# Performance work log

Measured on AMD Instinct MI355X. Metric: run time of the kernel, lower is better.

## Reference

```python
import jax, jax.numpy as jnp
import numpy as np

TOP_K = 2

def setup_inputs() -> dict:
    key = jax.random.key(0)
    ks = jax.random.split(key, 6)
    B, S, D, F, E = 2, 2048, 1024, 4096, 8
    sd = 1.0 / np.sqrt(D)
    sf = 1.0 / np.sqrt(F)
    return {
        "x": jax.random.normal(ks[0], (B, S, D), jnp.float32),
        "gate_w": jax.random.normal(ks[1], (D, E), jnp.float32) * sd,
        "w1": jax.random.normal(ks[2], (E, D, F), jnp.float32) * sd,
        "b1": jax.random.normal(ks[3], (E, F), jnp.float32) * 0.01,
        "w2": jax.random.normal(ks[4], (E, F, D), jnp.float32) * sf,
        "b2": jax.random.normal(ks[5], (E, D), jnp.float32) * 0.01,
    }

def reference(x, gate_w, w1, b1, w2, b2):
    B, S, D = x.shape
    T = B * S
    xf = x.reshape(T, D)
    # gating: softmax over experts, top-k, renormalize
    gate_scores = jax.nn.softmax(xf @ gate_w, axis=-1)          # [T, E]
    topk_scores, topk_idx = jax.lax.top_k(gate_scores, TOP_K)    # [T, K]
    topk_scores = topk_scores / jnp.sum(topk_scores, axis=-1, keepdims=True)
    # all experts applied to all tokens (dense grouped FFN), exact erf GELU as nn.GELU
    h = jax.nn.gelu(jnp.einsum('td,edf->etf', xf, w1) + b1[:, None, :], approximate=False)  # [E,T,F]
    y = jnp.einsum('etf,efd->etd', h, w2) + b2[:, None, :]       # [E,T,D]
    # combine: gather the top-k expert outputs per token, weight and sum
    tok = jnp.arange(T)
    y_sel = y[topk_idx.T, tok[None, :]]                           # [K,T,D]
    out = jnp.einsum('kt,ktd->td', topk_scores.T, y_sel)
    return out.reshape(B, S, D)
```

## Files before the change

### kernel.cpp

```cpp
#include <hip/hip_runtime.h>
#include <hip/hip_bf16.h>
#include <stdint.h>

#define T_TOK 4096
#define D_DIM 1024
#define F_DIM 4096
#define E_NUM 8
#define NROUTED (T_TOK * 2)

typedef __attribute__((ext_vector_type(8))) __bf16 bf16x8;
typedef __attribute__((ext_vector_type(4))) float f32x4;

#define WS_COUNTS 0
#define WS_CURSORS 64
#define WS_OFFSETS 128
#define WS_TOPKI 4096
#define WS_TOPKW (WS_TOPKI + NROUTED * 4)
#define WS_ROWS (WS_TOPKW + NROUTED * 4)
#define WS_DEST (WS_ROWS + NROUTED * 4)
#define WS_XB ((size_t)1 << 20)
#define WS_W1T (WS_XB + (size_t)T_TOK * D_DIM * 2)
#define WS_W2T (WS_W1T + (size_t)E_NUM * D_DIM * F_DIM * 2)
#define WS_H (WS_W2T + (size_t)E_NUM * D_DIM * F_DIM * 2)
#define WS_Y (WS_H + (size_t)NROUTED * F_DIM * 2)

__device__ __forceinline__ unsigned short f2bf(float f) {
  uint32_t u = __float_as_uint(f);
  uint32_t r = (u + 0x7FFFu + ((u >> 16) & 1u)) >> 16;
  return (unsigned short)r;
}

__device__ __forceinline__ void gll16(const void* g, void* l) {
  __builtin_amdgcn_global_load_lds(
      (__attribute__((address_space(1))) void*)(void*)(g),
      (__attribute__((address_space(3))) void*)(l), 16, 0, 0);
}

__global__ void cast_x_kernel(const float* __restrict__ x, unsigned short* __restrict__ xb) {
  int n4 = T_TOK * D_DIM / 4;
  for (int i = blockIdx.x * blockDim.x + threadIdx.x; i < n4; i += gridDim.x * blockDim.x) {
    float4 v = reinterpret_cast<const float4*>(x)[i];
    ushort4 o;
    o.x = f2bf(v.x); o.y = f2bf(v.y); o.z = f2bf(v.z); o.w = f2bf(v.w);
    reinterpret_cast<ushort4*>(xb)[i] = o;
  }
}

__global__ void transpose_cast_kernel(const float* __restrict__ src,
                                      unsigned short* __restrict__ dst, int R, int C) {
  __shared__ float tile[32][33];
  const int e = blockIdx.z;
  const int c0 = blockIdx.x * 32, r0 = blockIdx.y * 32;
  const float* s = src + (size_t)e * R * C;
  unsigned short* d = dst + (size_t)e * C * R;
  const int t = threadIdx.x;
  const int lr = t >> 3, lc4 = t & 7;
  float4 v = *reinterpret_cast<const float4*>(s + (size_t)(r0 + lr) * C + c0 + lc4 * 4);
  tile[lr][lc4 * 4 + 0] = v.x; tile[lr][lc4 * 4 + 1] = v.y;
  tile[lr][lc4 * 4 + 2] = v.z; tile[lr][lc4 * 4 + 3] = v.w;
  __syncthreads();
  ushort4 o;
  o.x = f2bf(tile[lc4 * 4 + 0][lr]); o.y = f2bf(tile[lc4 * 4 + 1][lr]);
  o.z = f2bf(tile[lc4 * 4 + 2][lr]); o.w = f2bf(tile[lc4 * 4 + 3][lr]);
  *reinterpret_cast<ushort4*>(d + (size_t)(c0 + lr) * R + r0 + lc4 * 4) = o;
}

__global__ void gate_kernel(const float* __restrict__ x, const float* __restrict__ gw,
                            int* __restrict__ topk_i, float* __restrict__ topk_w,
                            int* __restrict__ counts) {
  const int wave = threadIdx.x >> 6, lane = threadIdx.x & 63;
  const int t = blockIdx.x * 4 + wave;
  const float* xr = x + (size_t)t * D_DIM;
  double acc[E_NUM] = {0, 0, 0, 0, 0, 0, 0, 0};
  for (int d = lane; d < D_DIM; d += 64) {
    double xv = (double)xr[d];
    const float* g = gw + d * E_NUM;
#pragma unroll
    for (int e = 0; e < E_NUM; e++) acc[e] += xv * (double)g[e];
  }
#pragma unroll
  for (int off = 32; off > 0; off >>= 1) {
#pragma unroll
    for (int e = 0; e < E_NUM; e++) acc[e] += __shfl_xor(acc[e], off, 64);
  }
  if (lane == 0) {
    int i0 = 0; double b0 = acc[0];
    for (int e = 1; e < E_NUM; e++) if (acc[e] > b0) { b0 = acc[e]; i0 = e; }
    int i1 = -1; double b1v = -1e300;
    for (int e = 0; e < E_NUM; e++) if (e != i0 && acc[e] > b1v) { b1v = acc[e]; i1 = e; }
    double w0 = 1.0 / (1.0 + exp(b1v - b0));
    topk_i[t * 2] = i0; topk_i[t * 2 + 1] = i1;
    topk_w[t * 2] = (float)w0; topk_w[t * 2 + 1] = (float)(1.0 - w0);
    atomicAdd(&counts[i0], 1); atomicAdd(&counts[i1], 1);
  }
}

__global__ void scan_kernel(const int* __restrict__ counts, int* __restrict__ offsets) {
  if (threadIdx.x == 0) {
    int s = 0;
    for (int e = 0; e < E_NUM; e++) { offsets[e] = s; s += counts[e]; }
  }
}

__global__ void build_lists_kernel(const int* __restrict__ topk_i, const int* __restrict__ offsets,
                                   int* __restrict__ cursors, int* __restrict__ rows,
                                   int* __restrict__ dest) {
  int t = blockIdx.x * blockDim.x + threadIdx.x;
  if (t >= T_TOK) return;
#pragma unroll
  for (int k = 0; k < 2; k++) {
    int e = topk_i[t * 2 + k];
    int slot = atomicAdd(&cursors[e], 1);
    int r = offsets[e] + slot;
    rows[r] = t;
    dest[t * 2 + k] = r;
  }
}

__global__ __launch_bounds__(256, 2) void gemm1_kernel(
    const unsigned short* __restrict__ xb, const unsigned short* __restrict__ w1T,
    const float* __restrict__ b1, const int* __restrict__ counts,
    const int* __restrict__ offsets, const int* __restrict__ rows,
    unsigned short* __restrict__ h) {
  const int e = blockIdx.z;
  const int cnt = counts[e];
  const int mt = blockIdx.y;
  if (mt * 128 >= cnt) return;
  const int nt = blockIdx.x;
  const int off = offsets[e];
  const int t = threadIdx.x;
  const int lane = t & 63, wave = t >> 6;
  const int wm = wave >> 1, wn = wave & 1;

  __shared__ __align__(16) unsigned short ldsA[2][4096];
  __shared__ __align__(16) unsigned short ldsB[2][4096];

  const int tr = t >> 2, tc = t & 3;
  const int a0 = mt * 128 + tr;
  const int a1 = a0 + 64;
  const int g0 = rows[off + min(a0, cnt - 1)];
  const int g1 = rows[off + min(a1, cnt - 1)];
  const unsigned short* aptr0 = xb + (size_t)g0 * D_DIM + tc * 8;
  const unsigned short* aptr1 = xb + (size_t)g1 * D_DIM + tc * 8;
  const unsigned short* wb = w1T + (size_t)e * F_DIM * D_DIM;
  const unsigned short* bptr0 = wb + (size_t)(nt * 128 + tr) * D_DIM + tc * 8;
  const unsigned short* bptr1 = bptr0 + (size_t)64 * D_DIM;

  f32x4 acc[4][4];
  const f32x4 z = {0.f, 0.f, 0.f, 0.f};
#pragma unroll
  for (int i = 0; i < 4; i++)
#pragma unroll
    for (int j = 0; j < 4; j++) acc[i][j] = z;

  auto stage = [&](int buf, int kt) {
    const int kb = kt * 32;
    gll16(aptr0 + kb, &ldsA[buf][wave * 512]);
    gll16(aptr1 + kb, &ldsA[buf][2048 + wave * 512]);
    gll16(bptr0 + kb, &ldsB[buf][wave * 512]);
    gll16(bptr1 + kb, &ldsB[buf][2048 + wave * 512]);
  };
  stage(0, 0);
  asm volatile("s_waitcnt vmcnt(0)" ::: "memory");
  __syncthreads();

  const int rA = wm * 64 + (lane & 15);
  const int rB = wn * 64 + (lane & 15);
  const int ko = (lane >> 4) * 8;
  const int NK = D_DIM / 32;

  for (int kt = 0; kt < NK; ++kt) {
    const int cur = kt & 1;
    if (kt + 1 < NK) stage(cur ^ 1, kt + 1);
    bf16x8 af[4], bfr[4];
#pragma unroll
    for (int mf = 0; mf < 4; mf++)
      af[mf] = *(const bf16x8*)&ldsA[cur][(rA + mf * 16) * 32 + ko];
#pragma unroll
    for (int nf = 0; nf < 4; nf++)
      bfr[nf] = *(const bf16x8*)&ldsB[cur][(rB + nf * 16) * 32 + ko];
#pragma unroll
    for (int mf = 0; mf < 4; mf++)
#pragma unroll
      for (int nf = 0; nf < 4; nf++)
        acc[mf][nf] = __builtin_amdgcn_mfma_f32_16x16x32_bf16(af[mf], bfr[nf], acc[mf][nf], 0, 0, 0);
    asm volatile("s_waitcnt vmcnt(0)" ::: "memory");
    __syncthreads();
  }

  const int valid = cnt - mt * 128;
  const int col = lane & 15;
  const int rq = (lane >> 4) * 4;
#pragma unroll
  for (int nf = 0; nf < 4; nf++) {
    const int c = nt * 128 + wn * 64 + nf * 16 + col;
    const float bias = b1[(size_t)e * F_DIM + c];
#pragma unroll
    for (int mf = 0; mf < 4; mf++) {
#pragma unroll
      for (int r4 = 0; r4 < 4; r4++) {
        int rloc = wm * 64 + mf * 16 + rq + r4;
        if (rloc < valid) {
          float v = acc[mf][nf][r4] + bias;
          v = 0.5f * v * (1.0f + erff(v * 0.7071067811865475f));
          h[(size_t)(off + mt * 128 + rloc) * F_DIM + c] = f2bf(v);
        }
      }
    }
  }
}

__global__ __launch_bounds__(256, 2) void gemm2_kernel(
    const unsigned short* __restrict__ h, const unsigned short* __restrict__ w2T,
    const float* __restrict__ b2, const int* __restrict__ counts,
    const int* __restrict__ offsets, float* __restrict__ y) {
  const int e = blockIdx.z;
  const int cnt = counts[e];
  const int mt = blockIdx.y;
  if (mt * 128 >= cnt) return;
  const int nt = blockIdx.x;
  const int off = offsets[e];
  const int t = threadIdx.x;
  const int lane = t & 63, wave = t >> 6;
  const int wm = wave >> 1, wn = wave & 1;

  __shared__ __align__(16) unsigned short ldsA[2][4096];
  __shared__ __align__(16) unsigned short ldsB[2][4096];

  const int tr = t >> 2, tc = t & 3;
  const int l0 = min(mt * 128 + tr, cnt - 1);
  const int l1 = min(mt * 128 + 64 + tr, cnt - 1);
  const unsigned short* aptr0 = h + (size_t)(off + l0) * F_DIM + tc * 8;
  const unsigned short* aptr1 = h + (size_t)(off + l1) * F_DIM + tc * 8;
  const unsigned short* wb = w2T + (size_t)e * D_DIM * F_DIM;
  const unsigned short* bptr0 = wb + (size_t)(nt * 128 + tr) * F_DIM + tc * 8;
  const unsigned short* bptr1 = bptr0 + (size_t)64 * F_DIM;

  f32x4 acc[4][4];
  const f32x4 z = {0.f, 0.f, 0.f, 0.f};
#pragma unroll
  for (int i = 0; i < 4; i++)
#pragma unroll
    for (int j = 0; j < 4; j++) acc[i][j] = z;

  auto stage = [&](int buf, int kt) {
    const int kb = kt * 32;
    gll16(aptr0 + kb, &ldsA[buf][wave * 512]);
    gll16(aptr1 + kb, &ldsA[buf][2048 + wave * 512]);
    gll16(bptr0 + kb, &ldsB[buf][wave * 512]);
    gll16(bptr1 + kb, &ldsB[buf][2048 + wave * 512]);
  };
  stage(0, 0);
  asm volatile("s_waitcnt vmcnt(0)" ::: "memory");
  __syncthreads();

  const int rA = wm * 64 + (lane & 15);
  const int rB = wn * 64 + (lane & 15);
  const int ko = (lane >> 4) * 8;
  const int NK = F_DIM / 32;

  for (int kt = 0; kt < NK; ++kt) {
    const int cur = kt & 1;
    if (kt + 1 < NK) stage(cur ^ 1, kt + 1);
    bf16x8 af[4], bfr[4];
#pragma unroll
    for (int mf = 0; mf < 4; mf++)
      af[mf] = *(const bf16x8*)&ldsA[cur][(rA + mf * 16) * 32 + ko];
#pragma unroll
    for (int nf = 0; nf < 4; nf++)
      bfr[nf] = *(const bf16x8*)&ldsB[cur][(rB + nf * 16) * 32 + ko];
#pragma unroll
    for (int mf = 0; mf < 4; mf++)
#pragma unroll
      for (int nf = 0; nf < 4; nf++)
        acc[mf][nf] = __builtin_amdgcn_mfma_f32_16x16x32_bf16(af[mf], bfr[nf], acc[mf][nf], 0, 0, 0);
    asm volatile("s_waitcnt vmcnt(0)" ::: "memory");
    __syncthreads();
  }

  const int valid = cnt - mt * 128;
  const int col = lane & 15;
  const int rq = (lane >> 4) * 4;
#pragma unroll
  for (int nf = 0; nf < 4; nf++) {
    const int c = nt * 128 + wn * 64 + nf * 16 + col;
    const float bias = b2[(size_t)e * D_DIM + c];
#pragma unroll
    for (int mf = 0; mf < 4; mf++) {
#pragma unroll
      for (int r4 = 0; r4 < 4; r4++) {
        int rloc = wm * 64 + mf * 16 + rq + r4;
        if (rloc < valid)
          y[(size_t)(off + mt * 128 + rloc) * D_DIM + c] = acc[mf][nf][r4] + bias;
      }
    }
  }
}

__global__ void combine_kernel(const float* __restrict__ y, const int* __restrict__ dest,
                               const float* __restrict__ tw, float* __restrict__ out) {
  const int n4 = T_TOK * D_DIM / 4;
  for (int i = blockIdx.x * blockDim.x + threadIdx.x; i < n4; i += gridDim.x * blockDim.x) {
    int tok = i >> 8;
    int c = i & 255;
    int r0 = dest[2 * tok], r1 = dest[2 * tok + 1];
    float w0 = tw[2 * tok], w1 = tw[2 * tok + 1];
    float4 a = reinterpret_cast<const float4*>(y + (size_t)r0 * D_DIM)[c];
    float4 b = reinterpret_cast<const float4*>(y + (size_t)r1 * D_DIM)[c];
    float4 o;
    o.x = w0 * a.x + w1 * b.x; o.y = w0 * a.y + w1 * b.y;
    o.z = w0 * a.z + w1 * b.z; o.w = w0 * a.w + w1 * b.w;
    reinterpret_cast<float4*>(out + (size_t)tok * D_DIM)[c] = o;
  }
}

extern "C" void kernel_launch(void* const* d_in, const int* in_sizes, int n_in,
                              void* d_out, int out_size, void* d_ws, size_t ws_size,
                              hipStream_t stream) {
  (void)in_sizes; (void)n_in; (void)out_size; (void)ws_size;
  const float* x = (const float*)d_in[0];
  const float* gw = (const float*)d_in[1];
  const float* w1 = (const float*)d_in[2];
  const float* b1 = (const float*)d_in[3];
  const float* w2 = (const float*)d_in[4];
  const float* b2 = (const float*)d_in[5];
  float* out = (float*)d_out;
  char* ws = (char*)d_ws;

  int* counts = (int*)(ws + WS_COUNTS);
  int* cursors = (int*)(ws + WS_CURSORS);
  int* offsets = (int*)(ws + WS_OFFSETS);
  int* topk_i = (int*)(ws + WS_TOPKI);
  float* topk_w = (float*)(ws + WS_TOPKW);
  int* rows = (int*)(ws + WS_ROWS);
  int* dest = (int*)(ws + WS_DEST);
  unsigned short* xb = (unsigned short*)(ws + WS_XB);
  unsigned short* w1T = (unsigned short*)(ws + WS_W1T);
  unsigned short* w2T = (unsigned short*)(ws + WS_W2T);
  unsigned short* hbuf = (unsigned short*)(ws + WS_H);
  float* ybuf = (float*)(ws + WS_Y);

  hipMemsetAsync(ws, 0, 4096, stream);
  cast_x_kernel<<<2048, 256, 0, stream>>>(x, xb);
  transpose_cast_kernel<<<dim3(F_DIM / 32, D_DIM / 32, E_NUM), 256, 0, stream>>>(w1, w1T, D_DIM, F_DIM);
  transpose_cast_kernel<<<dim3(D_DIM / 32, F_DIM / 32, E_NUM), 256, 0, stream>>>(w2, w2T, F_DIM, D_DIM);
  gate_kernel<<<T_TOK / 4, 256, 0, stream>>>(x, gw, topk_i, topk_w, counts);
  scan_kernel<<<1, 64, 0, stream>>>(counts, offsets);
  build_lists_kernel<<<T_TOK / 256, 256, 0, stream>>>(topk_i, offsets, cursors, rows, dest);
  gemm1_kernel<<<dim3(F_DIM / 128, 32, E_NUM), 256, 0, stream>>>(xb, w1T, b1, counts, offsets, rows, hbuf);
  gemm2_kernel<<<dim3(D_DIM / 128, 32, E_NUM), 256, 0, stream>>>(hbuf, w2T, b2, counts, offsets, ybuf);
  combine_kernel<<<2048, 256, 0, stream>>>(ybuf, dest, topk_w, out);
}
```

Before: 785.0 us.

## Triple-buffer GEMM pipelines, remap grid for XCD locality, widen transpose tiles

```diff
diff --git a/kernel.cpp b/kernel.cpp
--- a/kernel.cpp
+++ b/kernel.cpp
@@ -10,6 +10,7 @@
 
 typedef __attribute__((ext_vector_type(8))) __bf16 bf16x8;
 typedef __attribute__((ext_vector_type(4))) float f32x4;
+typedef __attribute__((ext_vector_type(8))) unsigned short u16x8;
 
 #define WS_COUNTS 0
 #define WS_CURSORS 64
@@ -48,21 +49,30 @@
 
 __global__ void transpose_cast_kernel(const float* __restrict__ src,
                                       unsigned short* __restrict__ dst, int R, int C) {
-  __shared__ float tile[32][33];
+  __shared__ float tile[64][65];
   const int e = blockIdx.z;
-  const int c0 = blockIdx.x * 32, r0 = blockIdx.y * 32;
+  const int c0 = blockIdx.x * 64, r0 = blockIdx.y * 64;
   const float* s = src + (size_t)e * R * C;
   unsigned short* d = dst + (size_t)e * C * R;
   const int t = threadIdx.x;
-  const int lr = t >> 3, lc4 = t & 7;
-  float4 v = *reinterpret_cast<const float4*>(s + (size_t)(r0 + lr) * C + c0 + lc4 * 4);
-  tile[lr][lc4 * 4 + 0] = v.x; tile[lr][lc4 * 4 + 1] = v.y;
-  tile[lr][lc4 * 4 + 2] = v.z; tile[lr][lc4 * 4 + 3] = v.w;
+  const int lr = t >> 4, lc = (t & 15) * 4;
+#pragma unroll
+  for (int rr = 0; rr < 4; rr++) {
+    const int r = lr + rr * 16;
+    float4 v = *reinterpret_cast<const float4*>(s + (size_t)(r0 + r) * C + c0 + lc);
+    tile[r][lc + 0] = v.x; tile[r][lc + 1] = v.y;
+    tile[r][lc + 2] = v.z; tile[r][lc + 3] = v.w;
+  }
   __syncthreads();
-  ushort4 o;
-  o.x = f2bf(tile[lc4 * 4 + 0][lr]); o.y = f2bf(tile[lc4 * 4 + 1][lr]);
-  o.z = f2bf(tile[lc4 * 4 + 2][lr]); o.w = f2bf(tile[lc4 * 4 + 3][lr]);
-  *reinterpret_cast<ushort4*>(d + (size_t)(c0 + lr) * R + r0 + lc4 * 4) = o;
+  const int wc = t >> 3, wr = (t & 7) * 8;
+#pragma unroll
+  for (int cc = 0; cc < 2; cc++) {
+    const int c = wc + cc * 32;
+    u16x8 o;
+#pragma unroll
+    for (int k = 0; k < 8; k++) o[k] = f2bf(tile[wr + k][c]);
+    *reinterpret_cast<u16x8*>(d + (size_t)(c0 + c) * R + r0 + wr) = o;
+  }
 }
 
 __global__ void gate_kernel(const float* __restrict__ x, const float* __restrict__ gw,
@@ -117,34 +127,42 @@
   }
 }
 
-__global__ __launch_bounds__(256, 2) void gemm1_kernel(
+__global__ __launch_bounds__(256, 3) void gemm1_kernel(
     const unsigned short* __restrict__ xb, const unsigned short* __restrict__ w1T,
     const float* __restrict__ b1, const int* __restrict__ counts,
     const int* __restrict__ offsets, const int* __restrict__ rows,
     unsigned short* __restrict__ h) {
-  const int e = blockIdx.z;
+  const int hw = blockIdx.x;
+  const int lid = (hw & 7) * (8192 >> 3) + (hw >> 3);
+  const int nt = lid & 31;
+  const int mt = (lid >> 5) & 31;
+  const int e = lid >> 10;
+
   const int cnt = counts[e];
-  const int mt = blockIdx.y;
   if (mt * 128 >= cnt) return;
-  const int nt = blockIdx.x;
   const int off = offsets[e];
   const int t = threadIdx.x;
   const int lane = t & 63, wave = t >> 6;
   const int wm = wave >> 1, wn = wave & 1;
 
-  __shared__ __align__(16) unsigned short ldsA[2][4096];
-  __shared__ __align__(16) unsigned short ldsB[2][4096];
+  __shared__ __align__(16) unsigned short ldsA[3][4096];
+  __shared__ __align__(16) unsigned short ldsB[3][4096];
 
   const int tr = t >> 2, tc = t & 3;
   const int a0 = mt * 128 + tr;
-  const int a1 = a0 + 64;
   const int g0 = rows[off + min(a0, cnt - 1)];
-  const int g1 = rows[off + min(a1, cnt - 1)];
+  const int g1 = rows[off + min(a0 + 64, cnt - 1)];
   const unsigned short* aptr0 = xb + (size_t)g0 * D_DIM + tc * 8;
   const unsigned short* aptr1 = xb + (size_t)g1 * D_DIM + tc * 8;
   const unsigned short* wb = w1T + (size_t)e * F_DIM * D_DIM;
   const unsigned short* bptr0 = wb + (size_t)(nt * 128 + tr) * D_DIM + tc * 8;
   const unsigned short* bptr1 = bptr0 + (size_t)64 * D_DIM;
+
+  const int col = lane & 15;
+  float bias_v[4];
+#pragma unroll
+  for (int nf = 0; nf < 4; nf++)
+    bias_v[nf] = b1[(size_t)e * F_DIM + nt * 128 + wn * 64 + nf * 16 + col];
 
   f32x4 acc[4][4];
   const f32x4 z = {0.f, 0.f, 0.f, 0.f};
@@ -160,9 +178,10 @@
     gll16(bptr0 + kb, &ldsB[buf][wave * 512]);
     gll16(bptr1 + kb, &ldsB[buf][2048 + wave * 512]);
   };
+
+  asm volatile("s_waitcnt vmcnt(0)" ::: "memory");
   stage(0, 0);
-  asm volatile("s_waitcnt vmcnt(0)" ::: "memory");
-  __syncthreads();
+  stage(1, 1);
 
   const int rA = wm * 64 + (lane & 15);
   const int rB = wn * 64 + (lane & 15);
@@ -170,8 +189,16 @@
   const int NK = D_DIM / 32;
 
   for (int kt = 0; kt < NK; ++kt) {
-    const int cur = kt & 1;
-    if (kt + 1 < NK) stage(cur ^ 1, kt + 1);
+    const int cur = kt - (kt / 3) * 3;
+    if (kt + 2 < NK) {
+      stage((kt + 2) - ((kt + 2) / 3) * 3, kt + 2);
+      asm volatile("s_waitcnt vmcnt(8)" ::: "memory");
+    } else if (kt + 2 == NK) {
+      asm volatile("s_waitcnt vmcnt(4)" ::: "memory");
+    } else {
+      asm volatile("s_waitcnt vmcnt(0)" ::: "memory");
+    }
+    __builtin_amdgcn_s_barrier();
     bf16x8 af[4], bfr[4];
 #pragma unroll
     for (int mf = 0; mf < 4; mf++)
@@ -184,17 +211,15 @@
 #pragma unroll
       for (int nf = 0; nf < 4; nf++)
         acc[mf][nf] = __builtin_amdgcn_mfma_f32_16x16x32_bf16(af[mf], bfr[nf], acc[mf][nf], 0, 0, 0);
-    asm volatile("s_waitcnt vmcnt(0)" ::: "memory");
-    __syncthreads();
+    __builtin_amdgcn_s_barrier();
   }
 
   const int valid = cnt - mt * 128;
-  const int col = lane & 15;
   const int rq = (lane >> 4) * 4;
 #pragma unroll
   for (int nf = 0; nf < 4; nf++) {
     const int c = nt * 128 + wn * 64 + nf * 16 + col;
-    const float bias = b1[(size_t)e * F_DIM + c];
+    const float bias = bias_v[nf];
 #pragma unroll
     for (int mf = 0; mf < 4; mf++) {
 #pragma unroll
@@ -210,22 +235,25 @@
   }
 }
 
-__global__ __launch_bounds__(256, 2) void gemm2_kernel(
+__global__ __launch_bounds__(256, 3) void gemm2_kernel(
     const unsigned short* __restrict__ h, const unsigned short* __restrict__ w2T,
     const float* __restrict__ b2, const int* __restrict__ counts,
     const int* __restrict__ offsets, float* __restrict__ y) {
-  const int e = blockIdx.z;
+  const int hw = blockIdx.x;
+  const int lid = (hw & 7) * (2048 >> 3) + (hw >> 3);
+  const int nt = lid & 7;
+  const int mt = (lid >> 3) & 31;
+  const int e = lid >> 8;
+
   const int cnt = counts[e];
-  const int mt = blockIdx.y;
   if (mt * 128 >= cnt) return;
-  const int nt = blockIdx.x;
   const int off = offsets[e];
   const int t = threadIdx.x;
   const int lane = t & 63, wave = t >> 6;
   const int wm = wave >> 1, wn = wave & 1;
 
-  __shared__ __align__(16) unsigned short ldsA[2][4096];
-  __shared__ __align__(16) unsigned short ldsB[2][4096];
+  __shared__ __align__(16) unsigned short ldsA[3][4096];
+  __shared__ __align__(16) unsigned short ldsB[3][4096];
 
   const int tr = t >> 2, tc = t & 3;
   const int l0 = min(mt * 128 + tr, cnt - 1);
@@ -236,6 +264,12 @@
   const unsigned short* bptr0 = wb + (size_t)(nt * 128 + tr) * F_DIM + tc * 8;
   const unsigned short* bptr1 = bptr0 + (size_t)64 * F_DIM;
 
+  const int col = lane & 15;
+  float bias_v[4];
+#pragma unroll
+  for (int nf = 0; nf < 4; nf++)
+    bias_v[nf] = b2[(size_t)e * D_DIM + nt * 128 + wn * 64 + nf * 16 + col];
+
   f32x4 acc[4][4];
   const f32x4 z = {0.f, 0.f, 0.f, 0.f};
 #pragma unroll
@@ -250,9 +284,10 @@
     gll16(bptr0 + kb, &ldsB[buf][wave * 512]);
     gll16(bptr1 + kb, &ldsB[buf][2048 + wave * 512]);
   };
+
+  asm volatile("s_waitcnt vmcnt(0)" ::: "memory");
   stage(0, 0);
-  asm volatile("s_waitcnt vmcnt(0)" ::: "memory");
-  __syncthreads();
+  stage(1, 1);
 
   const int rA = wm * 64 + (lane & 15);
   const int rB = wn * 64 + (lane & 15);
@@ -260,8 +295,16 @@
   const int NK = F_DIM / 32;
 
   for (int kt = 0; kt < NK; ++kt) {
-    const int cur = kt & 1;
-    if (kt + 1 < NK) stage(cur ^ 1, kt + 1);
+    const int cur = kt - (kt / 3) * 3;
+    if (kt + 2 < NK) {
+      stage((kt + 2) - ((kt + 2) / 3) * 3, kt + 2);
+      asm volatile("s_waitcnt vmcnt(8)" ::: "memory");
+    } else if (kt + 2 == NK) {
+      asm volatile("s_waitcnt vmcnt(4)" ::: "memory");
+    } else {
+      asm volatile("s_waitcnt vmcnt(0)" ::: "memory");
+    }
+    __builtin_amdgcn_s_barrier();
     bf16x8 af[4], bfr[4];
 #pragma unroll
     for (int mf = 0; mf < 4; mf++)
@@ -274,17 +317,15 @@
 #pragma unroll
       for (int nf = 0; nf < 4; nf++)
         acc[mf][nf] = __builtin_amdgcn_mfma_f32_16x16x32_bf16(af[mf], bfr[nf], acc[mf][nf], 0, 0, 0);
-    asm volatile("s_waitcnt vmcnt(0)" ::: "memory");
-    __syncthreads();
+    __builtin_amdgcn_s_barrier();
   }
 
   const int valid = cnt - mt * 128;
-  const int col = lane & 15;
   const int rq = (lane >> 4) * 4;
 #pragma unroll
   for (int nf = 0; nf < 4; nf++) {
     const int c = nt * 128 + wn * 64 + nf * 16 + col;
-    const float bias = b2[(size_t)e * D_DIM + c];
+    const float bias = bias_v[nf];
 #pragma unroll
     for (int mf = 0; mf < 4; mf++) {
 #pragma unroll
@@ -342,12 +383,12 @@
 
   hipMemsetAsync(ws, 0, 4096, stream);
   cast_x_kernel<<<2048, 256, 0, stream>>>(x, xb);
-  transpose_cast_kernel<<<dim3(F_DIM / 32, D_DIM / 32, E_NUM), 256, 0, stream>>>(w1, w1T, D_DIM, F_DIM);
-  transpose_cast_kernel<<<dim3(D_DIM / 32, F_DIM / 32, E_NUM), 256, 0, stream>>>(w2, w2T, F_DIM, D_DIM);
   gate_kernel<<<T_TOK / 4, 256, 0, stream>>>(x, gw, topk_i, topk_w, counts);
   scan_kernel<<<1, 64, 0, stream>>>(counts, offsets);
   build_lists_kernel<<<T_TOK / 256, 256, 0, stream>>>(topk_i, offsets, cursors, rows, dest);
-  gemm1_kernel<<<dim3(F_DIM / 128, 32, E_NUM), 256, 0, stream>>>(xb, w1T, b1, counts, offsets, rows, hbuf);
-  gemm2_kernel<<<dim3(D_DIM / 128, 32, E_NUM), 256, 0, stream>>>(hbuf, w2T, b2, counts, offsets, ybuf);
+  transpose_cast_kernel<<<dim3(F_DIM / 64, D_DIM / 64, E_NUM), 256, 0, stream>>>(w1, w1T, D_DIM, F_DIM);
+  gemm1_kernel<<<8192, 256, 0, stream>>>(xb, w1T, b1, counts, offsets, rows, hbuf);
+  transpose_cast_kernel<<<dim3(D_DIM / 64, F_DIM / 64, E_NUM), 256, 0, stream>>>(w2, w2T, F_DIM, D_DIM);
+  gemm2_kernel<<<2048, 256, 0, stream>>>(hbuf, w2T, b2, counts, offsets, ybuf);
   combine_kernel<<<2048, 256, 0, stream>>>(ybuf, dest, topk_w, out);
 }
```

Result: faster. 702.6 us (-10.5%).
